# Performance work log

Hardware: AMD Instinct MI355X
Metric: run time of the kernel (lower is better)

Reference implementation:

```python
import jax, jax.numpy as jnp
import numpy as np
import math

D = 2048  # hidden_size
B, S = 4, 2048
EPS = 1e-5


def _ln(z, g, b):
    m = jnp.mean(z, axis=-1, keepdims=True)
    v = jnp.mean(jnp.square(z - m), axis=-1, keepdims=True)
    return (z - m) * jax.lax.rsqrt(v + EPS) * g + b


def _rotate_half(x):
    h = x.shape[-1] // 2
    return jnp.concatenate([-x[..., h:], x[..., :h]], axis=-1)


def _mas_normalize(logits):
    m = jnp.max(jnp.abs(logits), axis=-1, keepdims=True)
    return logits / (m + 1e-9)


def setup_inputs() -> dict:
    key = jax.random.key(0)
    ks = jax.random.split(key, 12)
    std = 0.02
    return {
        "x": jax.random.normal(ks[0], (B, S, D), dtype=jnp.float32),
        "position_ids": jnp.arange(S, dtype=jnp.int32),
        "ln1_g": jnp.ones((D,), jnp.float32),
        "ln1_b": jnp.zeros((D,), jnp.float32),
        # stacked params for [q, k, v, o]
        "mu_w": std * jax.random.normal(ks[1], (4, D, D), dtype=jnp.float32),
        "mu_b": jnp.zeros((4, D), jnp.float32),
        "proto_w": std * jax.random.normal(ks[2], (4, D, D), dtype=jnp.float32),
        "gate": jnp.zeros((4, D), jnp.float32),
        "pt_w": std * jax.random.normal(ks[3], (4, D, D), dtype=jnp.float32),
        "pln_g": jnp.ones((4, D), jnp.float32),
        "pln_b": jnp.zeros((4, D), jnp.float32),
        "incoming": std * jax.random.normal(ks[4], (4, D, D), dtype=jnp.float32),
    }


def reference(x, position_ids, ln1_g, ln1_b, mu_w, mu_b, proto_w, gate,
              pt_w, pln_g, pln_b, incoming):
    d = x.shape[-1]
    inv_sqrt_d = 1.0 / math.sqrt(d)

    # proto_state = proto_weight + LN(Linear(incoming))  per module [4, D, D]
    prc = jnp.einsum('nij,noj->nio', incoming, pt_w)
    proto_state = proto_w + _ln(prc, pln_g[:, None, :], pln_b[:, None, :])

    ln1_out = _ln(x, ln1_g, ln1_b)            # [B,S,D]
    ctx = jnp.mean(ln1_out, axis=1)           # [B,D]

    # qkv computation outputs: silu(ln1_out @ mu_w.T + mu_b) for n in {q,k,v}
    comp = jax.nn.silu(jnp.einsum('bsd,nod->nbso', ln1_out, mu_w[:3])
                       + mu_b[:3][:, None, None, :])            # [3,B,S,D]
    # routing from context vector
    match_ctx = jnp.einsum('bd,nod->nbo', ctx, proto_state[:3]) * inv_sqrt_d
    routing = match_ctx + gate[:3][:, None, :]                  # [3,B,D]
    gating = _mas_normalize(routing)
    masked = gating[:, :, None, :] * comp                       # [3,B,S,D]
    q, k, v = masked[0], masked[1], masked[2]

    # RoPE over full hidden dim (num_heads == 1)
    seq = position_ids.shape[0]
    inv_freq = 1.0 / (10000.0 ** (jnp.arange(0, d, 2, dtype=jnp.float32) / d))
    t = jnp.arange(seq, dtype=jnp.float32)
    freqs = t[:, None] * inv_freq[None, :]
    emb = jnp.concatenate([freqs, freqs], axis=-1)              # [S,D]
    cos = jnp.cos(emb)[position_ids]
    sin = jnp.sin(emb)[position_ids]
    q = q * cos + _rotate_half(q) * sin
    k = k * cos + _rotate_half(k) * sin

    # causal single-head attention, scale 1/sqrt(head_dim=D)
    scores = jnp.einsum('bqd,bkd->bqk', q, k) * inv_sqrt_d      # [B,S,S]
    causal = jnp.tril(jnp.ones((seq, seq), dtype=bool))
    scores = jnp.where(causal, scores, jnp.finfo(scores.dtype).min)
    probs = jax.nn.softmax(scores, axis=-1)
    attn_out = jnp.einsum('bqk,bkd->bqd', probs, v)             # [B,S,D]

    # output SPL + routing
    ctx_o = jnp.mean(attn_out, axis=1)
    c_o = jax.nn.silu(jnp.einsum('bsd,od->bso', attn_out, mu_w[3]) + mu_b[3])
    match_o = jnp.einsum('bd,od->bo', ctx_o, proto_state[3]) * inv_sqrt_d
    gating_o = _mas_normalize(match_o + gate[3])
    x_out = x + gating_o[:, None, :] * c_o
    return x_out
```

## Files before the change

### kernel.cpp

```cpp
#include <hip/hip_runtime.h>
#include <hip/hip_bf16.h>
#include <hip/hip_fp16.h>

#define Dh 2048
#define Bh 4
#define Sh 2048
#define NROW 8192
#define HALF 1024
#define INV_SQRT_D 0.022097086912079608f
#define LNEPS 1e-5f

typedef __hip_bfloat16 bf16;
typedef short short8 __attribute__((ext_vector_type(8)));
typedef float f32x4 __attribute__((ext_vector_type(4)));

__device__ inline float warp_sum(float x) {
#pragma unroll
  for (int o = 32; o > 0; o >>= 1) x += __shfl_down(x, o);
  return x;
}
__device__ inline float warp_max(float x) {
#pragma unroll
  for (int o = 32; o > 0; o >>= 1) x = fmaxf(x, __shfl_down(x, o));
  return x;
}
__device__ inline float block_sum(float x, float* sm4) {
  x = warp_sum(x);
  int w = threadIdx.x >> 6;
  if ((threadIdx.x & 63) == 0) sm4[w] = x;
  __syncthreads();
  float r = sm4[0] + sm4[1] + sm4[2] + sm4[3];
  __syncthreads();
  return r;
}
__device__ inline float block_max(float x, float* sm4) {
  x = warp_max(x);
  int w = threadIdx.x >> 6;
  if ((threadIdx.x & 63) == 0) sm4[w] = x;
  __syncthreads();
  float r = fmaxf(fmaxf(sm4[0], sm4[1]), fmaxf(sm4[2], sm4[3]));
  __syncthreads();
  return r;
}

__device__ inline void gload_lds16(const void* g, void* lds) {
  __builtin_amdgcn_global_load_lds(
      (const __attribute__((address_space(1))) unsigned int*)(unsigned long long)g,
      (__attribute__((address_space(3))) unsigned int*)(unsigned long long)lds,
      16, 0, 0);
}

#define MM(R, AF)                                                              \
  acc[R][0] = __builtin_amdgcn_mfma_f32_16x16x32_bf16(AF, b0, acc[R][0], 0, 0, 0); \
  acc[R][1] = __builtin_amdgcn_mfma_f32_16x16x32_bf16(AF, b1, acc[R][1], 0, 0, 0); \
  acc[R][2] = __builtin_amdgcn_mfma_f32_16x16x32_bf16(AF, b2, acc[R][2], 0, 0, 0); \
  acc[R][3] = __builtin_amdgcn_mfma_f32_16x16x32_bf16(AF, b3, acc[R][3], 0, 0, 0);

template <int MODE>
__global__ __launch_bounds__(512) void pgemm(
    const bf16* __restrict__ Aall, const bf16* __restrict__ Ball,
    void* __restrict__ Call, int N, int K, int lda, int ldb,
    long sAz, long sBz, long sCz,
    const float* __restrict__ e0, const float* __restrict__ e1,
    const float* __restrict__ e2) {
  const int bm0 = blockIdx.x * 256;
  const int bn0 = blockIdx.y * 256;
  if (MODE == 2 && bn0 > bm0 + 255) return;
  const int z = blockIdx.z;
  const bf16* A = Aall + (long)z * sAz;
  const bf16* B = Ball + (long)z * sBz;

  __shared__ __align__(16) char smem[65536];
  const int tid = threadIdx.x;
  const int l = tid & 63, w = tid >> 6;
  const int wr = w >> 2, wc = w & 3;

  f32x4 acc[8][4] = {};
  const int nt = K >> 5;

  const int sg = (((l & 3) ^ ((l >> 3) & 3)) << 3);
  const int srow = (w << 4) + (l >> 2);
  const bf16* aS0 = A + (long)(bm0 + srow) * lda + sg;
  const bf16* aS1 = A + (long)(bm0 + 128 + srow) * lda + sg;
  const bf16* bS0 = B + (long)(bn0 + srow) * ldb + sg;
  const bf16* bS1 = B + (long)(bn0 + 128 + srow) * ldb + sg;
  char* const dA = smem + (w << 10);
  char* const dB = smem + 16384 + (w << 10);

  auto stageA = [&](int tt) {
    int boff = (tt & 1) << 15;
    gload_lds16(aS0 + (tt << 5), dA + boff);
    gload_lds16(aS1 + (tt << 5), dA + boff + 8192);
  };
  auto stageB = [&](int tt) {
    int boff = (tt & 1) << 15;
    gload_lds16(bS0 + (tt << 5), dB + boff);
    gload_lds16(bS1 + (tt << 5), dB + boff + 8192);
  };

  stageA(0); stageB(0);
  if (nt > 1) stageB(1);
  if (nt > 1) asm volatile("s_waitcnt vmcnt(2)" ::: "memory");
  else        asm volatile("s_waitcnt vmcnt(0)" ::: "memory");
  __builtin_amdgcn_sched_barrier(0);
  asm volatile("s_barrier" ::: "memory");

  const int rslot = (((l >> 4) ^ ((l >> 1) & 3)) << 4);
  const int abyte = (((wr << 7) + (l & 15)) << 6) + rslot;
  const int bbyte = (((wc << 6) + (l & 15)) << 6) + rslot;

  for (int t = 0; t < nt; ++t) {
    const char* Ab = smem + ((t & 1) << 15);
    const char* Bb = Ab + 16384;
    short8 b0 = *(const short8*)(Bb + bbyte);
    short8 b1 = *(const short8*)(Bb + bbyte + 1024);
    short8 b2 = *(const short8*)(Bb + bbyte + 2048);
    short8 b3 = *(const short8*)(Bb + bbyte + 3072);
    short8 a0 = *(const short8*)(Ab + abyte);
    short8 a1 = *(const short8*)(Ab + abyte + 1024);
    short8 a2 = *(const short8*)(Ab + abyte + 2048);
    short8 a3 = *(const short8*)(Ab + abyte + 3072);
    if (t + 1 < nt) stageA(t + 1);
    MM(0, a0) MM(1, a1) MM(2, a2) MM(3, a3)
    asm volatile("s_waitcnt lgkmcnt(0)" ::: "memory");
    asm volatile("s_barrier" ::: "memory");
    short8 a4 = *(const short8*)(Ab + abyte + 4096);
    short8 a5 = *(const short8*)(Ab + abyte + 5120);
    short8 a6 = *(const short8*)(Ab + abyte + 6144);
    short8 a7 = *(const short8*)(Ab + abyte + 7168);
    if (t + 2 < nt) stageB(t + 2);
    MM(4, a4) MM(5, a5) MM(6, a6) MM(7, a7)
    if (t < nt - 1) {
      asm volatile("s_waitcnt lgkmcnt(0)" ::: "memory");
      if (t + 2 < nt) asm volatile("s_waitcnt vmcnt(2)" ::: "memory");
      else            asm volatile("s_waitcnt vmcnt(0)" ::: "memory");
      __builtin_amdgcn_sched_barrier(0);
      asm volatile("s_barrier" ::: "memory");
    }
  }

  const int lc = l & 15, lr4 = (l >> 4) << 2;
#pragma unroll
  for (int fr = 0; fr < 8; ++fr) {
    int gr0 = bm0 + (wr << 7) + fr * 16 + lr4;
#pragma unroll
    for (int fc = 0; fc < 4; ++fc) {
      int gc = bn0 + (wc << 6) + fc * 16 + lc;
#pragma unroll
      for (int qv = 0; qv < 4; ++qv) {
        int gr = gr0 + qv;
        float a = acc[fr][fc][qv];
        if (MODE == 0) {
          ((float*)Call + (long)z * sCz)[(long)gr * N + gc] = a;
        } else if (MODE == 1) {
          float val = a + e0[z * Dh + gc];
          float sil = val / (1.f + __expf(-val));
          int bb = gr >> 11;
          float g = e1[(z * Bh + bb) * Dh + gc];
          ((bf16*)Call + (long)z * sCz)[(long)gr * N + gc] =
              __float2bfloat16(sil * g);
        } else if (MODE == 2) {
          ((__half*)Call + (long)z * sCz)[(long)gr * N + gc] =
              __float2half(a * INV_SQRT_D);
        } else {
          float val = a + e0[gc];
          float sil = val / (1.f + __expf(-val));
          int bb = gr >> 11;
          ((float*)Call)[(long)gr * N + gc] =
              e2[(long)gr * N + gc] + e1[bb * Dh + gc] * sil;
        }
      }
    }
  }
}

__global__ __launch_bounds__(512) void pgemm_h(
    const bf16* __restrict__ Aall, const bf16* __restrict__ Ball,
    bf16* __restrict__ Call, int N, int lda, int ldb,
    long sAz, long sBz, long sCz) {
  const int fid = blockIdx.x;
  const int p = fid >> 8, q = fid & 255;
  const int mh = q >> 5;
  const int z = (q >> 3) & 3, ni = q & 7;
  const int mi = p ? (15 - mh) : mh;
  const int bm0 = mi * 128, bn0 = ni * 256;
  const bf16* A = Aall + (long)z * sAz;
  const bf16* B = Ball + (long)z * sBz;

  __shared__ __align__(16) char smem[49152];
  const int tid = threadIdx.x;
  const int l = tid & 63, w = tid >> 6;
  const int wr = w >> 2, wc = w & 3;
  f32x4 acc[4][4] = {};
  const int nt = (bm0 + 128) >> 5;

  const int sg = (((l & 3) ^ ((l >> 3) & 3)) << 3);
  const int srow = (w << 4) + (l >> 2);
  const bf16* aS  = A + (long)(bm0 + srow) * lda + sg;
  const bf16* bS0 = B + (long)(bn0 + srow) * ldb + sg;
  const bf16* bS1 = B + (long)(bn0 + 128 + srow) * ldb + sg;
  char* const dA = smem + (w << 10);
  char* const dB = smem + 8192 + (w << 10);

  auto stageA = [&](int tt) {
    gload_lds16(aS + (tt << 5), dA + (tt & 1) * 24576);
  };
  auto stageB = [&](int tt) {
    int boff = (tt & 1) * 24576;
    gload_lds16(bS0 + (tt << 5), dB + boff);
    gload_lds16(bS1 + (tt << 5), dB + boff + 8192);
  };

  stageA(0); stageB(0);
  if (nt > 1) stageB(1);
  if (nt > 1) asm volatile("s_waitcnt vmcnt(2)" ::: "memory");
  else        asm volatile("s_waitcnt vmcnt(0)" ::: "memory");
  __builtin_amdgcn_sched_barrier(0);
  asm volatile("s_barrier" ::: "memory");

  const int rslot = (((l >> 4) ^ ((l >> 1) & 3)) << 4);
  const int abyte = (((wr << 6) + (l & 15)) << 6) + rslot;
  const int bbyte = (((wc << 6) + (l & 15)) << 6) + rslot;

  for (int t = 0; t < nt; ++t) {
    const char* Ab = smem + (t & 1) * 24576;
    const char* Bb = Ab + 8192;
    short8 b0 = *(const short8*)(Bb + bbyte);
    short8 b1 = *(const short8*)(Bb + bbyte + 1024);
    short8 b2 = *(const short8*)(Bb + bbyte + 2048);
    short8 b3 = *(const short8*)(Bb + bbyte + 3072);
    short8 a0 = *(const short8*)(Ab + abyte);
    short8 a1 = *(const short8*)(Ab + abyte + 1024);
    if (t + 1 < nt) stageA(t + 1);
    MM(0, a0) MM(1, a1)
    asm volatile("s_waitcnt lgkmcnt(0)" ::: "memory");
    asm volatile("s_barrier" ::: "memory");
    short8 a2 = *(const short8*)(Ab + abyte + 2048);
    short8 a3 = *(const short8*)(Ab + abyte + 3072);
    if (t + 2 < nt) stageB(t + 2);
    MM(2, a2) MM(3, a3)
    if (t < nt - 1) {
      asm volatile("s_waitcnt lgkmcnt(0)" ::: "memory");
      if (t + 2 < nt) asm volatile("s_waitcnt vmcnt(2)" ::: "memory");
      else            asm volatile("s_waitcnt vmcnt(0)" ::: "memory");
      __builtin_amdgcn_sched_barrier(0);
      asm volatile("s_barrier" ::: "memory");
    }
  }

  const int lc = l & 15, lr4 = (l >> 4) << 2;
  bf16* C = Call + (long)z * sCz;
#pragma unroll
  for (int fr = 0; fr < 4; ++fr) {
    int gr0 = bm0 + (wr << 6) + fr * 16 + lr4;
#pragma unroll
    for (int fc = 0; fc < 4; ++fc) {
      int gc = bn0 + (wc << 6) + fc * 16 + lc;
#pragma unroll
      for (int qv = 0; qv < 4; ++qv)
        C[(long)(gr0 + qv) * N + gc] = __float2bfloat16(acc[fr][fc][qv]);
    }
  }
}

__global__ __launch_bounds__(256) void cvt3_kernel(
    const float* __restrict__ s0, const float* __restrict__ s1,
    const float* __restrict__ s2, bf16* __restrict__ o0, bf16* __restrict__ o1,
    bf16* __restrict__ o2, long n) {
  const float* in = (blockIdx.y == 0) ? s0 : (blockIdx.y == 1) ? s1 : s2;
  bf16* out = (blockIdx.y == 0) ? o0 : (blockIdx.y == 1) ? o1 : o2;
  long i = ((long)blockIdx.x * 256 + threadIdx.x) * 4;
  if (i >= n) return;
  float4 v = *(const float4*)(in + i);
  out[i + 0] = __float2bfloat16(v.x);
  out[i + 1] = __float2bfloat16(v.y);
  out[i + 2] = __float2bfloat16(v.z);
  out[i + 3] = __float2bfloat16(v.w);
}

__global__ __launch_bounds__(256) void transpose_kernel(const bf16* __restrict__ in,
                                                        bf16* __restrict__ out) {
  __shared__ bf16 t[64][65];
  int b = blockIdx.z;
  int s0 = blockIdx.x * 64, d0 = blockIdx.y * 64;
  const bf16* ib = in + (long)b * Sh * Dh;
  bf16* ob = out + (long)b * Sh * Dh;
  int tx = threadIdx.x & 63, ty = threadIdx.x >> 6;
#pragma unroll
  for (int r = ty; r < 64; r += 4) t[r][tx] = ib[(long)(s0 + r) * Dh + d0 + tx];
  __syncthreads();
#pragma unroll
  for (int r = ty; r < 64; r += 4) ob[(long)(d0 + r) * Sh + s0 + tx] = t[tx][r];
}

__global__ __launch_bounds__(256) void ln1_kernel(const float* __restrict__ x,
    const float* __restrict__ g, const float* __restrict__ b, bf16* __restrict__ out) {
  __shared__ float sm4[4];
  long r = blockIdx.x;
  const float* row = x + r * Dh;
  float v[8];
  float s = 0.f, s2 = 0.f;
#pragma unroll
  for (int c = 0; c < 8; ++c) {
    float t = row[threadIdx.x + c * 256];
    v[c] = t; s += t; s2 += t * t;
  }
  s = block_sum(s, sm4);
  s2 = block_sum(s2, sm4);
  float mean = s * (1.f / Dh);
  float rstd = rsqrtf(s2 * (1.f / Dh) - mean * mean + LNEPS);
#pragma unroll
  for (int c = 0; c < 8; ++c) {
    int o = threadIdx.x + c * 256;
    out[r * Dh + o] = __float2bfloat16((v[c] - mean) * rstd * g[o] + b[o]);
  }
}

__global__ __launch_bounds__(256) void meanrow_kernel(const bf16* __restrict__ in,
                                                      float* __restrict__ outbd) {
  int gid = blockIdx.x * 256 + threadIdx.x;
  int s0 = blockIdx.y * 128;
  long base = ((long)(gid >> 11) * Sh + s0) * Dh + (gid & 2047);
  float s = 0.f;
  for (int t = 0; t < 128; ++t) s += __bfloat162float(in[base + (long)t * Dh]);
  atomicAdd(&outbd[gid], s * (1.f / Sh));
}

__global__ __launch_bounds__(256) void route_kernel(
    const float* __restrict__ prc, const float* __restrict__ proto_w,
    const float* __restrict__ pln_g, const float* __restrict__ pln_b,
    const float* __restrict__ gate, const float* __restrict__ ctx,
    float* __restrict__ routing, float* __restrict__ ps3) {
  __shared__ float sm4[4];
  int i = blockIdx.x, n = blockIdx.y;
  long rb = ((long)n * Dh + i) * Dh;
  float v[8];
  float s = 0.f, s2 = 0.f;
#pragma unroll
  for (int c = 0; c < 8; ++c) {
    float t = prc[rb + threadIdx.x + c * 256];
    v[c] = t; s += t; s2 += t * t;
  }
  s = block_sum(s, sm4);
  s2 = block_sum(s2, sm4);
  float mean = s * (1.f / Dh);
  float rstd = rsqrtf(s2 * (1.f / Dh) - mean * mean + LNEPS);
  if (n == 3) {
#pragma unroll
    for (int c = 0; c < 8; ++c) {
      int o = threadIdx.x + c * 256;
      float ps = proto_w[rb + o] + (v[c] - mean) * rstd * pln_g[3 * Dh + o] + pln_b[3 * Dh + o];
      ps3[(long)i * Dh + o] = ps;
    }
  } else {
    float acc[4] = {0.f, 0.f, 0.f, 0.f};
#pragma unroll
    for (int c = 0; c < 8; ++c) {
      int o = threadIdx.x + c * 256;
      float ps = proto_w[rb + o] + (v[c] - mean) * rstd * pln_g[n * Dh + o] + pln_b[n * Dh + o];
#pragma unroll
      for (int b = 0; b < 4; ++b) acc[b] += ps * ctx[b * Dh + o];
    }
    for (int b = 0; b < 4; ++b) {
      float r = block_sum(acc[b], sm4);
      if (threadIdx.x == 0)
        routing[(n * 4 + b) * Dh + i] = r * INV_SQRT_D + gate[n * Dh + i];
    }
  }
}

__global__ __launch_bounds__(256) void route_o_kernel(
    const float* __restrict__ ps3, const float* __restrict__ ctxo,
    const float* __restrict__ gate, float* __restrict__ routing) {
  __shared__ float sm4[4];
  int i = blockIdx.x;
  float acc[4] = {0.f, 0.f, 0.f, 0.f};
#pragma unroll
  for (int c = 0; c < 8; ++c) {
    int o = threadIdx.x + c * 256;
    float p = ps3[(long)i * Dh + o];
#pragma unroll
    for (int b = 0; b < 4; ++b) acc[b] += p * ctxo[b * Dh + o];
  }
  for (int b = 0; b < 4; ++b) {
    float r = block_sum(acc[b], sm4);
    if (threadIdx.x == 0)
      routing[(12 + b) * Dh + i] = r * INV_SQRT_D + gate[3 * Dh + i];
  }
}

__global__ __launch_bounds__(256) void masnorm_kernel(const float* __restrict__ rin,
                                                      float* __restrict__ gout) {
  __shared__ float sm4[4];
  long r = blockIdx.x;
  float m = 0.f;
#pragma unroll
  for (int c = 0; c < 8; ++c)
    m = fmaxf(m, fabsf(rin[r * Dh + threadIdx.x + c * 256]));
  m = block_max(m, sm4);
  float inv = 1.f / (m + 1e-9f);
#pragma unroll
  for (int c = 0; c < 8; ++c) {
    int o = threadIdx.x + c * 256;
    gout[r * Dh + o] = rin[r * Dh + o] * inv;
  }
}

__global__ __launch_bounds__(256) void rope_table_kernel(float* __restrict__ cosT,
                                                         float* __restrict__ sinT) {
  int idx = blockIdx.x * 256 + threadIdx.x;
  int t = idx >> 10, f = idx & 1023;
  float inv_freq = expf(-(float)f * (9.210340371976184f / 1024.f));
  float ang = (float)t * inv_freq;
  cosT[idx] = cosf(ang);
  sinT[idx] = sinf(ang);
}

__global__ __launch_bounds__(256) void rope_kernel(bf16* __restrict__ q, bf16* __restrict__ k,
    const int* __restrict__ pos, const float* __restrict__ cosT,
    const float* __restrict__ sinT) {
  long r = blockIdx.x;
  int s = (int)(r & (Sh - 1));
  int p = pos[s];
#pragma unroll
  for (int c = 0; c < 4; ++c) {
    int t = threadIdx.x + c * 256;
    float cv = cosT[(long)p * HALF + t];
    float sv = sinT[(long)p * HALF + t];
    long i1 = r * Dh + t, i2 = i1 + HALF;
    float q1 = __bfloat162float(q[i1]), q2 = __bfloat162float(q[i2]);
    q[i1] = __float2bfloat16(q1 * cv - q2 * sv);
    q[i2] = __float2bfloat16(q2 * cv + q1 * sv);
    float k1 = __bfloat162float(k[i1]), k2 = __bfloat162float(k[i2]);
    k[i1] = __float2bfloat16(k1 * cv - k2 * sv);
    k[i2] = __float2bfloat16(k2 * cv + k1 * sv);
  }
}

__global__ __launch_bounds__(256) void softmax_kernel(const __half* __restrict__ scores,
                                                      bf16* __restrict__ probs) {
  __shared__ float buf[Sh];
  __shared__ float sm4[4];
  long r = blockIdx.x;
  int qi = (int)(r & (Sh - 1));
  const __half* row = scores + r * (long)Sh;
  bf16* prow = probs + r * (long)Sh;
  int n = qi + 1;
  float m = -3.0e38f;
  for (int o = threadIdx.x; o < n; o += 256) {
    float x = __half2float(row[o]); buf[o] = x; m = fmaxf(m, x);
  }
  m = block_max(m, sm4);
  float s = 0.f;
  for (int o = threadIdx.x; o < n; o += 256) {
    float e = __expf(buf[o] - m); buf[o] = e; s += e;
  }
  s = block_sum(s, sm4);
  float inv = 1.f / s;
  for (int o = threadIdx.x; o < n; o += 256) prow[o] = __float2bfloat16(buf[o] * inv);
  for (int o = n + (int)threadIdx.x; o < Sh; o += 256) prow[o] = __float2bfloat16(0.f);
}

extern "C" void kernel_launch(void* const* d_in, const int* in_sizes, int n_in,
                              void* d_out, int out_size, void* d_ws, size_t ws_size,
                              hipStream_t stream) {
  const float* x       = (const float*)d_in[0];
  const int*   pos     = (const int*)d_in[1];
  const float* ln1_g   = (const float*)d_in[2];
  const float* ln1_b   = (const float*)d_in[3];
  const float* mu_w    = (const float*)d_in[4];
  const float* mu_b    = (const float*)d_in[5];
  const float* proto_w = (const float*)d_in[6];
  const float* gate    = (const float*)d_in[7];
  const float* pt_w    = (const float*)d_in[8];
  const float* pln_g   = (const float*)d_in[9];
  const float* pln_b   = (const float*)d_in[10];
  const float* incoming= (const float*)d_in[11];

  char* w = (char*)d_ws;
  const long BF = 33554432L;
  bf16*  ln1    = (bf16*)(w);
  bf16*  qb     = (bf16*)(w + BF);
  bf16*  kb     = (bf16*)(w + 2 * BF);
  bf16*  vb     = (bf16*)(w + 3 * BF);
  bf16*  attn   = (bf16*)(w + 4 * BF);
  bf16*  mu_wb  = (bf16*)(w + 5 * BF);
  bf16*  ptw_b  = (bf16*)(w + 6 * BF);
  bf16*  vT     = ptw_b;
  bf16*  inc_b  = (bf16*)(w + 7 * BF);
  bf16*  probs  = inc_b;
  float* ps3    = (float*)(w + 8 * BF);
  float* cosT   = (float*)(w + 8 * BF + 16777216L);
  float* sinT   = cosT + (long)Sh * HALF;
  float* ctx    = sinT + (long)Sh * HALF;
  float* ctxo   = ctx + Bh * Dh;
  float* routing= ctxo + Bh * Dh;
  float* gating = routing + 16 * Dh;
  float*  prc    = (float*)d_out;
  __half* scores = (__half*)d_out;

  const long DD4 = 4L * Dh * Dh;

  hipMemsetAsync(ctx, 0, 2L * Bh * Dh * sizeof(float), stream);

  rope_table_kernel<<<(Sh * HALF) / 256, 256, 0, stream>>>(cosT, sinT);
  cvt3_kernel<<<dim3(DD4 / 1024, 3), 256, 0, stream>>>(
      mu_w, incoming, pt_w, mu_wb, inc_b, ptw_b, DD4);
  ln1_kernel<<<NROW, 256, 0, stream>>>(x, ln1_g, ln1_b, ln1);
  meanrow_kernel<<<dim3(32, 16), 256, 0, stream>>>(ln1, ctx);
  pgemm<0><<<dim3(8, 8, 4), 512, 0, stream>>>(
      inc_b, ptw_b, prc, Dh, Dh, Dh, Dh,
      (long)Dh * Dh, (long)Dh * Dh, (long)Dh * Dh, nullptr, nullptr, nullptr);
  route_kernel<<<dim3(Dh, 4), 256, 0, stream>>>(prc, proto_w, pln_g, pln_b,
                                                gate, ctx, routing, ps3);
  masnorm_kernel<<<12, 256, 0, stream>>>(routing, gating);
  pgemm<1><<<dim3(32, 8, 3), 512, 0, stream>>>(
      ln1, mu_wb, qb, Dh, Dh, Dh, Dh,
      0L, (long)Dh * Dh, (long)NROW * Dh, mu_b, gating, nullptr);
  rope_kernel<<<NROW, 256, 0, stream>>>(qb, kb, pos, cosT, sinT);
  pgemm<2><<<dim3(8, 8, 4), 512, 0, stream>>>(
      qb, kb, scores, Sh, Dh, Dh, Dh,
      (long)Sh * Dh, (long)Sh * Dh, (long)Sh * Sh, nullptr, nullptr, nullptr);
  softmax_kernel<<<Bh * Sh, 256, 0, stream>>>(scores, probs);
  transpose_kernel<<<dim3(32, 32, 4), 256, 0, stream>>>(vb, vT);
  pgemm_h<<<512, 512, 0, stream>>>(
      probs, vT, attn, Dh, Sh, Sh,
      (long)Sh * Sh, (long)Dh * Sh, (long)Sh * Dh);
  meanrow_kernel<<<dim3(32, 16), 256, 0, stream>>>(attn, ctxo);
  route_o_kernel<<<Dh, 256, 0, stream>>>(ps3, ctxo, gate, routing);
  masnorm_kernel<<<4, 256, 0, stream>>>(routing + 12 * Dh, gating + 12 * Dh);
  pgemm<4><<<dim3(32, 8, 1), 512, 0, stream>>>(
      attn, mu_wb + 3L * Dh * Dh, d_out, Dh, Dh, Dh, Dh,
      0L, 0L, 0L, mu_b + 3 * Dh, gating + 12 * Dh, x);
}
```

Baseline: 663.9 us.

## Double GEMM K-tile to 64 and vectorize layernorm and softmax loads/stores

```diff
diff --git a/kernel.cpp b/kernel.cpp
--- a/kernel.cpp
+++ b/kernel.cpp
@@ -13,6 +13,14 @@
 typedef __hip_bfloat16 bf16;
 typedef short short8 __attribute__((ext_vector_type(8)));
 typedef float f32x4 __attribute__((ext_vector_type(4)));
+typedef unsigned short ushort8v __attribute__((ext_vector_type(8)));
+typedef unsigned short ushort4v __attribute__((ext_vector_type(4)));
+
+__device__ inline float h2f_bits(unsigned short u) {
+  __half h;
+  *(unsigned short*)&h = u;
+  return __half2float(h);
+}
 
 __device__ inline float warp_sum(float x) {
 #pragma unroll
@@ -50,11 +58,11 @@
       16, 0, 0);
 }
 
-#define MM(R, AF)                                                              \
-  acc[R][0] = __builtin_amdgcn_mfma_f32_16x16x32_bf16(AF, b0, acc[R][0], 0, 0, 0); \
-  acc[R][1] = __builtin_amdgcn_mfma_f32_16x16x32_bf16(AF, b1, acc[R][1], 0, 0, 0); \
-  acc[R][2] = __builtin_amdgcn_mfma_f32_16x16x32_bf16(AF, b2, acc[R][2], 0, 0, 0); \
-  acc[R][3] = __builtin_amdgcn_mfma_f32_16x16x32_bf16(AF, b3, acc[R][3], 0, 0, 0);
+#define MM4(R, AF, B0, B1, B2, B3)                                             \
+  acc[R][0] = __builtin_amdgcn_mfma_f32_16x16x32_bf16(AF, B0, acc[R][0], 0, 0, 0); \
+  acc[R][1] = __builtin_amdgcn_mfma_f32_16x16x32_bf16(AF, B1, acc[R][1], 0, 0, 0); \
+  acc[R][2] = __builtin_amdgcn_mfma_f32_16x16x32_bf16(AF, B2, acc[R][2], 0, 0, 0); \
+  acc[R][3] = __builtin_amdgcn_mfma_f32_16x16x32_bf16(AF, B3, acc[R][3], 0, 0, 0);
 
 template <int MODE>
 __global__ __launch_bounds__(512) void pgemm(
@@ -70,69 +78,95 @@
   const bf16* A = Aall + (long)z * sAz;
   const bf16* B = Ball + (long)z * sBz;
 
-  __shared__ __align__(16) char smem[65536];
+  __shared__ __align__(16) char smem[131072];
   const int tid = threadIdx.x;
   const int l = tid & 63, w = tid >> 6;
   const int wr = w >> 2, wc = w & 3;
 
   f32x4 acc[8][4] = {};
-  const int nt = K >> 5;
-
-  const int sg = (((l & 3) ^ ((l >> 3) & 3)) << 3);
-  const int srow = (w << 4) + (l >> 2);
+  const int nt = K >> 6;
+
+  const int sg = (((l & 7) ^ ((l >> 3) & 7)) << 3);
+  const int srow = (w << 3) + (l >> 3);
   const bf16* aS0 = A + (long)(bm0 + srow) * lda + sg;
-  const bf16* aS1 = A + (long)(bm0 + 128 + srow) * lda + sg;
-  const bf16* bS0 = B + (long)(bn0 + srow) * ldb + sg;
-  const bf16* bS1 = B + (long)(bn0 + 128 + srow) * ldb + sg;
+  const bf16* aS1 = A + (long)(bm0 + 64 + srow) * lda + sg;
+  const bf16* aS2 = A + (long)(bm0 + 128 + srow) * lda + sg;
+  const bf16* aS3 = A + (long)(bm0 + 192 + srow) * lda + sg;
+  const bf16* bT0 = B + (long)(bn0 + srow) * ldb + sg;
+  const bf16* bT1 = B + (long)(bn0 + 64 + srow) * ldb + sg;
+  const bf16* bT2 = B + (long)(bn0 + 128 + srow) * ldb + sg;
+  const bf16* bT3 = B + (long)(bn0 + 192 + srow) * ldb + sg;
   char* const dA = smem + (w << 10);
-  char* const dB = smem + 16384 + (w << 10);
+  char* const dB = smem + 65536 + (w << 10);
 
   auto stageA = [&](int tt) {
     int boff = (tt & 1) << 15;
-    gload_lds16(aS0 + (tt << 5), dA + boff);
-    gload_lds16(aS1 + (tt << 5), dA + boff + 8192);
+    gload_lds16(aS0 + (tt << 6), dA + boff);
+    gload_lds16(aS1 + (tt << 6), dA + boff + 8192);
+    gload_lds16(aS2 + (tt << 6), dA + boff + 16384);
+    gload_lds16(aS3 + (tt << 6), dA + boff + 24576);
   };
   auto stageB = [&](int tt) {
     int boff = (tt & 1) << 15;
-    gload_lds16(bS0 + (tt << 5), dB + boff);
-    gload_lds16(bS1 + (tt << 5), dB + boff + 8192);
+    gload_lds16(bT0 + (tt << 6), dB + boff);
+    gload_lds16(bT1 + (tt << 6), dB + boff + 8192);
+    gload_lds16(bT2 + (tt << 6), dB + boff + 16384);
+    gload_lds16(bT3 + (tt << 6), dB + boff + 24576);
   };
 
   stageA(0); stageB(0);
   if (nt > 1) stageB(1);
-  if (nt > 1) asm volatile("s_waitcnt vmcnt(2)" ::: "memory");
+  if (nt > 1) asm volatile("s_waitcnt vmcnt(4)" ::: "memory");
   else        asm volatile("s_waitcnt vmcnt(0)" ::: "memory");
   __builtin_amdgcn_sched_barrier(0);
   asm volatile("s_barrier" ::: "memory");
 
-  const int rslot = (((l >> 4) ^ ((l >> 1) & 3)) << 4);
-  const int abyte = (((wr << 7) + (l & 15)) << 6) + rslot;
-  const int bbyte = (((wc << 6) + (l & 15)) << 6) + rslot;
+  const int rslot = (((l >> 4) ^ (l & 7)) << 4);
+  const int abyte = (((wr << 7) + (l & 15)) << 7) + rslot;
+  const int bbyte = (((wc << 6) + (l & 15)) << 7) + rslot;
 
   for (int t = 0; t < nt; ++t) {
     const char* Ab = smem + ((t & 1) << 15);
-    const char* Bb = Ab + 16384;
-    short8 b0 = *(const short8*)(Bb + bbyte);
-    short8 b1 = *(const short8*)(Bb + bbyte + 1024);
-    short8 b2 = *(const short8*)(Bb + bbyte + 2048);
-    short8 b3 = *(const short8*)(Bb + bbyte + 3072);
+    const char* Bb = smem + 65536 + ((t & 1) << 15);
+    short8 b00 = *(const short8*)(Bb + bbyte);
+    short8 b01 = *(const short8*)(Bb + bbyte + 2048);
+    short8 b02 = *(const short8*)(Bb + bbyte + 4096);
+    short8 b03 = *(const short8*)(Bb + bbyte + 6144);
+    short8 b10 = *(const short8*)(Bb + (bbyte ^ 64));
+    short8 b11 = *(const short8*)(Bb + ((bbyte + 2048) ^ 64));
+    short8 b12 = *(const short8*)(Bb + ((bbyte + 4096) ^ 64));
+    short8 b13 = *(const short8*)(Bb + ((bbyte + 6144) ^ 64));
     short8 a0 = *(const short8*)(Ab + abyte);
-    short8 a1 = *(const short8*)(Ab + abyte + 1024);
-    short8 a2 = *(const short8*)(Ab + abyte + 2048);
-    short8 a3 = *(const short8*)(Ab + abyte + 3072);
+    short8 a1 = *(const short8*)(Ab + abyte + 2048);
+    short8 a2 = *(const short8*)(Ab + abyte + 4096);
+    short8 a3 = *(const short8*)(Ab + abyte + 6144);
+    short8 a4 = *(const short8*)(Ab + abyte + 8192);
+    short8 a5 = *(const short8*)(Ab + abyte + 10240);
+    short8 a6 = *(const short8*)(Ab + abyte + 12288);
+    short8 a7 = *(const short8*)(Ab + abyte + 14336);
     if (t + 1 < nt) stageA(t + 1);
-    MM(0, a0) MM(1, a1) MM(2, a2) MM(3, a3)
+    MM4(0, a0, b00, b01, b02, b03) MM4(1, a1, b00, b01, b02, b03)
+    MM4(2, a2, b00, b01, b02, b03) MM4(3, a3, b00, b01, b02, b03)
+    MM4(4, a4, b00, b01, b02, b03) MM4(5, a5, b00, b01, b02, b03)
+    MM4(6, a6, b00, b01, b02, b03) MM4(7, a7, b00, b01, b02, b03)
     asm volatile("s_waitcnt lgkmcnt(0)" ::: "memory");
     asm volatile("s_barrier" ::: "memory");
-    short8 a4 = *(const short8*)(Ab + abyte + 4096);
-    short8 a5 = *(const short8*)(Ab + abyte + 5120);
-    short8 a6 = *(const short8*)(Ab + abyte + 6144);
-    short8 a7 = *(const short8*)(Ab + abyte + 7168);
+    short8 c0 = *(const short8*)(Ab + (abyte ^ 64));
+    short8 c1 = *(const short8*)(Ab + ((abyte + 2048) ^ 64));
+    short8 c2 = *(const short8*)(Ab + ((abyte + 4096) ^ 64));
+    short8 c3 = *(const short8*)(Ab + ((abyte + 6144) ^ 64));
+    short8 c4 = *(const short8*)(Ab + ((abyte + 8192) ^ 64));
+    short8 c5 = *(const short8*)(Ab + ((abyte + 10240) ^ 64));
+    short8 c6 = *(const short8*)(Ab + ((abyte + 12288) ^ 64));
+    short8 c7 = *(const short8*)(Ab + ((abyte + 14336) ^ 64));
     if (t + 2 < nt) stageB(t + 2);
-    MM(4, a4) MM(5, a5) MM(6, a6) MM(7, a7)
+    MM4(0, c0, b10, b11, b12, b13) MM4(1, c1, b10, b11, b12, b13)
+    MM4(2, c2, b10, b11, b12, b13) MM4(3, c3, b10, b11, b12, b13)
+    MM4(4, c4, b10, b11, b12, b13) MM4(5, c5, b10, b11, b12, b13)
+    MM4(6, c6, b10, b11, b12, b13) MM4(7, c7, b10, b11, b12, b13)
     if (t < nt - 1) {
       asm volatile("s_waitcnt lgkmcnt(0)" ::: "memory");
-      if (t + 2 < nt) asm volatile("s_waitcnt vmcnt(2)" ::: "memory");
+      if (t + 2 < nt) asm volatile("s_waitcnt vmcnt(4)" ::: "memory");
       else            asm volatile("s_waitcnt vmcnt(0)" ::: "memory");
       __builtin_amdgcn_sched_barrier(0);
       asm volatile("s_barrier" ::: "memory");
@@ -174,6 +208,12 @@
   }
 }
 
+#define MM(R, AF)                                                              \
+  acc[R][0] = __builtin_amdgcn_mfma_f32_16x16x32_bf16(AF, b0, acc[R][0], 0, 0, 0); \
+  acc[R][1] = __builtin_amdgcn_mfma_f32_16x16x32_bf16(AF, b1, acc[R][1], 0, 0, 0); \
+  acc[R][2] = __builtin_amdgcn_mfma_f32_16x16x32_bf16(AF, b2, acc[R][2], 0, 0, 0); \
+  acc[R][3] = __builtin_amdgcn_mfma_f32_16x16x32_bf16(AF, b3, acc[R][3], 0, 0, 0);
+
 __global__ __launch_bounds__(512) void pgemm_h(
     const bf16* __restrict__ Aall, const bf16* __restrict__ Ball,
     bf16* __restrict__ Call, int N, int lda, int ldb,
@@ -298,22 +338,37 @@
   __shared__ float sm4[4];
   long r = blockIdx.x;
   const float* row = x + r * Dh;
-  float v[8];
-  float s = 0.f, s2 = 0.f;
-#pragma unroll
-  for (int c = 0; c < 8; ++c) {
-    float t = row[threadIdx.x + c * 256];
-    v[c] = t; s += t; s2 += t * t;
-  }
+  int i0 = threadIdx.x * 4, i1 = 1024 + threadIdx.x * 4;
+  float4 v0 = *(const float4*)(row + i0);
+  float4 v1 = *(const float4*)(row + i1);
+  float s = v0.x + v0.y + v0.z + v0.w + v1.x + v1.y + v1.z + v1.w;
+  float s2 = v0.x * v0.x + v0.y * v0.y + v0.z * v0.z + v0.w * v0.w +
+             v1.x * v1.x + v1.y * v1.y + v1.z * v1.z + v1.w * v1.w;
   s = block_sum(s, sm4);
   s2 = block_sum(s2, sm4);
   float mean = s * (1.f / Dh);
   float rstd = rsqrtf(s2 * (1.f / Dh) - mean * mean + LNEPS);
-#pragma unroll
-  for (int c = 0; c < 8; ++c) {
-    int o = threadIdx.x + c * 256;
-    out[r * Dh + o] = __float2bfloat16((v[c] - mean) * rstd * g[o] + b[o]);
-  }
+  float4 g0 = *(const float4*)(g + i0);
+  float4 g1 = *(const float4*)(g + i1);
+  float4 b0 = *(const float4*)(b + i0);
+  float4 b1 = *(const float4*)(b + i1);
+  ushort4v u0, u1;
+  {
+    bf16 t0 = __float2bfloat16((v0.x - mean) * rstd * g0.x + b0.x);
+    bf16 t1 = __float2bfloat16((v0.y - mean) * rstd * g0.y + b0.y);
+    bf16 t2 = __float2bfloat16((v0.z - mean) * rstd * g0.z + b0.z);
+    bf16 t3 = __float2bfloat16((v0.w - mean) * rstd * g0.w + b0.w);
+    u0[0] = *(unsigned short*)&t0; u0[1] = *(unsigned short*)&t1;
+    u0[2] = *(unsigned short*)&t2; u0[3] = *(unsigned short*)&t3;
+    bf16 s0b = __float2bfloat16((v1.x - mean) * rstd * g1.x + b1.x);
+    bf16 s1b = __float2bfloat16((v1.y - mean) * rstd * g1.y + b1.y);
+    bf16 s2b = __float2bfloat16((v1.z - mean) * rstd * g1.z + b1.z);
+    bf16 s3b = __float2bfloat16((v1.w - mean) * rstd * g1.w + b1.w);
+    u1[0] = *(unsigned short*)&s0b; u1[1] = *(unsigned short*)&s1b;
+    u1[2] = *(unsigned short*)&s2b; u1[3] = *(unsigned short*)&s3b;
+  }
+  *(ushort4v*)(out + r * Dh + i0) = u0;
+  *(ushort4v*)(out + r * Dh + i1) = u1;
 }
 
 __global__ __launch_bounds__(256) void meanrow_kernel(const bf16* __restrict__ in,
@@ -437,28 +492,50 @@
   }
 }
 
-__global__ __launch_bounds__(256) void softmax_kernel(const __half* __restrict__ scores,
+__global__ __launch_bounds__(256) void softmax_kernel(const unsigned short* __restrict__ scores,
                                                       bf16* __restrict__ probs) {
   __shared__ float buf[Sh];
   __shared__ float sm4[4];
   long r = blockIdx.x;
   int qi = (int)(r & (Sh - 1));
-  const __half* row = scores + r * (long)Sh;
+  const unsigned short* row = scores + r * (long)Sh;
   bf16* prow = probs + r * (long)Sh;
-  int n = qi + 1;
+  int tid = threadIdx.x;
+  int n = qi + 1, nv = n & ~7;
   float m = -3.0e38f;
-  for (int o = threadIdx.x; o < n; o += 256) {
-    float x = __half2float(row[o]); buf[o] = x; m = fmaxf(m, x);
+  for (int o = tid * 8; o < nv; o += 2048) {
+    ushort8v v = *(const ushort8v*)(row + o);
+#pragma unroll
+    for (int j = 0; j < 8; ++j) {
+      float x = h2f_bits(v[j]);
+      buf[o + j] = x;
+      m = fmaxf(m, x);
+    }
+  }
+  for (int o = nv + tid; o < n; o += 256) {
+    float x = h2f_bits(row[o]); buf[o] = x; m = fmaxf(m, x);
   }
   m = block_max(m, sm4);
   float s = 0.f;
-  for (int o = threadIdx.x; o < n; o += 256) {
+  for (int o = tid; o < n; o += 256) {
     float e = __expf(buf[o] - m); buf[o] = e; s += e;
   }
   s = block_sum(s, sm4);
   float inv = 1.f / s;
-  for (int o = threadIdx.x; o < n; o += 256) prow[o] = __float2bfloat16(buf[o] * inv);
-  for (int o = n + (int)threadIdx.x; o < Sh; o += 256) prow[o] = __float2bfloat16(0.f);
+  for (int o = tid * 8; o < nv; o += 2048) {
+    ushort8v u;
+#pragma unroll
+    for (int j = 0; j < 8; ++j) {
+      bf16 t = __float2bfloat16(buf[o + j] * inv);
+      u[j] = *(unsigned short*)&t;
+    }
+    *(ushort8v*)(prow + o) = u;
+  }
+  for (int o = nv + tid; o < n; o += 256) prow[o] = __float2bfloat16(buf[o] * inv);
+  int za = (n + 7) & ~7;
+  for (int o = n + tid; o < za && o < Sh; o += 256) prow[o] = __float2bfloat16(0.f);
+  ushort8v zz = {0, 0, 0, 0, 0, 0, 0, 0};
+  for (int o = za + tid * 8; o < Sh; o += 2048) *(ushort8v*)(prow + o) = zz;
 }
 
 extern "C" void kernel_launch(void* const* d_in, const int* in_sizes, int n_in,
@@ -521,7 +598,7 @@
   pgemm<2><<<dim3(8, 8, 4), 512, 0, stream>>>(
       qb, kb, scores, Sh, Dh, Dh, Dh,
       (long)Sh * Dh, (long)Sh * Dh, (long)Sh * Sh, nullptr, nullptr, nullptr);
-  softmax_kernel<<<Bh * Sh, 256, 0, stream>>>(scores, probs);
+  softmax_kernel<<<Bh * Sh, 256, 0, stream>>>((const unsigned short*)scores, probs);
   transpose_kernel<<<dim3(32, 32, 4), 256, 0, stream>>>(vb, vT);
   pgemm_h<<<512, 512, 0, stream>>>(
       probs, vT, attn, Dh, Sh, Sh,
```

Result: faster. 630.9 us (-5.0%).
